# Kernel tuning notes

Measured on AMD Instinct MI355X. Metric: run time of the kernel, lower is better.

## Reference

```python
import jax, jax.numpy as jnp
import numpy as np

H = 256  # hidden_size
B = 8192  # batch
S = 1024  # seq_length


def setup_inputs() -> dict:
    key = jax.random.key(0)
    ks = jax.random.split(key, 12)
    lim_g = 1.0 / np.sqrt(1 + H)  # torch Linear default init bound, fan_in = 1+H
    lim_o = 1.0 / np.sqrt(H)
    def lin(k, out_dim, in_dim, lim):
        kw, kb = jax.random.split(k)
        W = jax.random.uniform(kw, (out_dim, in_dim), jnp.float32, -lim, lim)
        b = jax.random.uniform(kb, (out_dim,), jnp.float32, -lim, lim)
        return W, b
    Wf, bf = lin(ks[0], H, 1 + H, lim_g)
    Wi, bi = lin(ks[1], H, 1 + H, lim_g)
    Wc, bc = lin(ks[2], H, 1 + H, lim_g)
    Wo, bo = lin(ks[3], H, 1 + H, lim_g)
    Wout, bout = lin(ks[4], 1, H, lim_o)
    x = jax.random.normal(ks[5], (B, S), jnp.float32)
    return {"x": x, "Wf": Wf, "bf": bf, "Wi": Wi, "bi": bi,
            "Wc": Wc, "bc": bc, "Wo": Wo, "bo": bo,
            "Wout": Wout, "bout": bout}


def reference(x, Wf, bf, Wi, bi, Wc, bc, Wo, bo, Wout, bout):
    B_, S_ = x.shape
    H_ = Wf.shape[0]
    # Fuse the four gate linears into one GEMM per step (same math):
    Wall = jnp.concatenate([Wf, Wi, Wc, Wo], axis=0)      # [4H, 1+H]
    ball = jnp.concatenate([bf, bi, bc, bo], axis=0)      # [4H]

    def step(carry, xt):
        h, c = carry                                       # [B,H], [B,H]
        conc = jnp.concatenate([xt[:, None], h], axis=1)   # [B, 1+H]
        g = conc @ Wall.T + ball                           # [B, 4H]
        f, i, cs, o = jnp.split(g, 4, axis=1)
        c = jax.nn.sigmoid(f) * c + jax.nn.sigmoid(i) * jnp.tanh(cs)
        h = jax.nn.sigmoid(o) * jnp.tanh(c)
        return (h, c), None

    h0 = jnp.zeros((B_, H_), x.dtype)
    c0 = jnp.zeros((B_, H_), x.dtype)
    (h, _), _ = jax.lax.scan(step, (h0, c0), x.T)          # scan over seq axis
    out = h @ Wout.T + bout                                # [B, 1]
    return out.squeeze(-1)                                 # [B]
```

## Files before the change

### kernel.cpp

```cpp
#include <hip/hip_runtime.h>
#include <hip/hip_fp16.h>


typedef _Float16 f16x8 __attribute__((ext_vector_type(8)));
typedef float f32x4 __attribute__((ext_vector_type(4)));
typedef unsigned int u32;
typedef unsigned short u16;

#define WINT_OFF 0u
#define W0B_OFF  524288u
#define FLAG_OFF 528384u
#define PUB_OFF  1048576u

static __device__ __forceinline__ float fast_exp2(float x) {
#if __has_builtin(__builtin_amdgcn_exp2f)
  return __builtin_amdgcn_exp2f(x);
#else
  return exp2f(x);
#endif
}
static __device__ __forceinline__ float fast_rcp(float x) {
#if __has_builtin(__builtin_amdgcn_rcpf)
  return __builtin_amdgcn_rcpf(x);
#else
  return 1.0f / x;
#endif
}
static __device__ __forceinline__ float fsig(float x) {
  return fast_rcp(1.0f + fast_exp2(-1.44269504f * x));
}
static __device__ __forceinline__ float ftanh_(float x) {
  float e = fast_exp2(2.88539008f * x);
  return 1.0f - 2.0f * fast_rcp(e + 1.0f);
}
static __device__ __forceinline__ u16 f16b(float f) {
  union { _Float16 h; u16 u; } cv; cv.h = (_Float16)f; return cv.u;
}
static __device__ __forceinline__ float h2f(u16 u) {
  union { u16 u; _Float16 h; } cv; cv.u = u; return (float)cv.h;
}
static __device__ __forceinline__ u16* pub_base(u16* pub, int set, int par,
                                                int pid, int half) {
  return pub + ((size_t)(((set * 2 + par) * 128 + pid) * 2 + half) << 12);
}

__global__ void lstm_prep(const float* __restrict__ Wf, const float* __restrict__ Wi,
                          const float* __restrict__ Wc, const float* __restrict__ Wo,
                          const float* __restrict__ bf_, const float* __restrict__ bi_,
                          const float* __restrict__ bc_, const float* __restrict__ bo_,
                          u16* __restrict__ Wint, u32* __restrict__ w0b) {
  int n = blockIdx.x;
  int k = threadIdx.x;
  int g = n >> 8, j = n & 255;
  const float* Ws = (g == 0) ? Wf : (g == 1) ? Wi : (g == 2) ? Wc : Wo;
  Wint[n * 256 + k] = f16b(Ws[j * 257 + 1 + k]);
  if (k == 0) {
    const float* bs = (g == 0) ? bf_ : (g == 1) ? bi_ : (g == 2) ? bc_ : bo_;
    w0b[n] = (u32)f16b(Ws[j * 257]) | ((u32)f16b(bs[j]) << 16);
  }
}

__global__ void lstm_zero(uint4* __restrict__ pub4, uint4* __restrict__ flags4,
                          float* __restrict__ out, const float* __restrict__ bout) {
  int idx = blockIdx.x * 256 + threadIdx.x;
  uint4 z = uint4{0, 0, 0, 0};
  if (idx < 131072) pub4[idx] = z;
  else if (idx < 262144) pub4[idx + 131072] = z;
  else if (idx < 264192) flags4[idx - 262144] = z;
  else { int o = idx - 264192; if (o < 8192) out[o] = bout[0]; }
}

__global__ __launch_bounds__(512, 2) void lstm_main(
    const u16* __restrict__ Wint, const u32* __restrict__ w0b,
    const float* __restrict__ x, const float* __restrict__ Wout,
    float* __restrict__ out, u16* __restrict__ pub, int* __restrict__ flags) {

  __shared__ __align__(16) u16 stg[2][2][4096];

  const int tid  = threadIdx.x;
  const int wv   = tid >> 6;
  const int lane = tid & 63;
  const int l15  = lane & 15;
  const int quad = lane >> 4;
  const int B    = blockIdx.x;
  const int mi   = (B >> 3) & 1;
  const int peer = B ^ 8;
  const int pid  = (B & 7) | ((B >> 4) << 3);
  const int rows0 = pid * 64;

  f16x8 wfrag[4][8];
#pragma unroll
  for (int g = 0; g < 4; ++g)
#pragma unroll
    for (int hm = 0; hm < 2; ++hm)
#pragma unroll
      for (int ktl = 0; ktl < 4; ++ktl) {
        int kbase = (hm == 0 ? mi : 1 - mi) * 128 + ktl * 32;
        wfrag[g][hm * 4 + ktl] = *(const f16x8*)(Wint +
            (size_t)(g * 256 + mi * 128 + wv * 16 + l15) * 256 + kbase + quad * 8);
      }
  uint4 w0bv[4];
#pragma unroll
  for (int g = 0; g < 4; ++g)
    w0bv[g] = *(const uint4*)(w0b + g * 256 + mi * 128 + wv * 16 + quad * 4);

#pragma unroll
  for (int i = 0; i < 4; ++i) ((uint4*)stg)[tid + i * 512] = uint4{0, 0, 0, 0};

  float cst[2][2][4];
#pragma unroll
  for (int s = 0; s < 2; ++s)
#pragma unroll
    for (int bt = 0; bt < 2; ++bt)
#pragma unroll
      for (int r = 0; r < 4; ++r) cst[s][bt][r] = 0.0f;

  const float* xq = x + (size_t)rows0 * 1024;
  float xcur[2][2];
#pragma unroll
  for (int s = 0; s < 2; ++s)
#pragma unroll
    for (int bt = 0; bt < 2; ++bt)
      xcur[s][bt] = xq[(size_t)(s * 32 + bt * 16 + l15) * 1024];

  int* const myflag = flags + B * 32;
  int* const pfl    = flags + peer * 32;

  __syncthreads();

#pragma unroll 1
  for (int t = 0; t < 1024; ++t) {
#pragma unroll
    for (int s = 0; s < 2; ++s) {
      f32x4 acc[4][2];
#pragma unroll
      for (int g = 0; g < 4; ++g) {
        u32 pka[4] = {w0bv[g].x, w0bv[g].y, w0bv[g].z, w0bv[g].w};
#pragma unroll
        for (int r = 0; r < 4; ++r) {
          float w0f = h2f((u16)pka[r]), bsf = h2f((u16)(pka[r] >> 16));
          acc[g][0][r] = xcur[s][0] * w0f + bsf;
          acc[g][1][r] = xcur[s][1] * w0f + bsf;
        }
      }
#pragma unroll
      for (int bt = 0; bt < 2; ++bt)
        xcur[s][bt] = xq[(size_t)(s * 32 + bt * 16 + l15) * 1024 + ((t + 1) & 1023)];

#pragma unroll
      for (int hm = 0; hm < 2; ++hm)
#pragma unroll
        for (int ktl = 0; ktl < 4; ++ktl) {
          f16x8 bb[2];
#pragma unroll
          for (int bt = 0; bt < 2; ++bt) {
            int b = bt * 16 + l15;
            int cp = (ktl * 4 + quad) ^ (b & 15);
            bb[bt] = *(const f16x8*)(&stg[s][hm][0] + b * 128 + cp * 8);
          }
#pragma unroll
          for (int g = 0; g < 4; ++g)
#pragma unroll
            for (int bt = 0; bt < 2; ++bt)
              acc[g][bt] = __builtin_amdgcn_mfma_f32_16x16x32_f16(
                  wfrag[g][hm * 4 + ktl], bb[bt], acc[g][bt], 0, 0, 0);
        }

      const int tn = (s == 0) ? t : t + 1;
      if (tn < 1024) {
        while (__hip_atomic_load(pfl + (s ^ 1) * 16, __ATOMIC_RELAXED,
                                 __HIP_MEMORY_SCOPE_AGENT) < tn)
          __builtin_amdgcn_s_sleep(1);
        const u16* srcO = pub_base(pub, s ^ 1, tn & 1, pid, mi);
        const u16* srcP = pub_base(pub, s ^ 1, tn & 1, pid, 1 - mi);
        __builtin_amdgcn_global_load_lds(
            (const __attribute__((address_space(1))) u32*)(srcO + wv * 512 + lane * 8),
            (__attribute__((address_space(3))) u32*)(&stg[s ^ 1][0][wv * 512]), 16, 0, 0);
        __builtin_amdgcn_global_load_lds(
            (const __attribute__((address_space(1))) u32*)(srcP + wv * 512 + lane * 8),
            (__attribute__((address_space(3))) u32*)(&stg[s ^ 1][1][wv * 512]), 16, 0, 0);
      }

      u16* pb = pub_base(pub, s, (t + 1) & 1, pid, mi);
#pragma unroll
      for (int bt = 0; bt < 2; ++bt) {
        int b = bt * 16 + l15;
        u32 lo, hi;
        {
          float h0, h1, h2, h3;
#pragma unroll
          for (int r = 0; r < 4; ++r) {
            float fg = acc[0][bt][r], ig = acc[1][bt][r];
            float cg = acc[2][bt][r], og = acc[3][bt][r];
            float c_ = fsig(fg) * cst[s][bt][r] + fsig(ig) * ftanh_(cg);
            cst[s][bt][r] = c_;
            float hv = fsig(og) * ftanh_(c_);
            if (r == 0) h0 = hv; else if (r == 1) h1 = hv;
            else if (r == 2) h2 = hv; else h3 = hv;
          }
          lo = (u32)f16b(h0) | ((u32)f16b(h1) << 16);
          hi = (u32)f16b(h2) | ((u32)f16b(h3) << 16);
        }
        int c16 = wv * 2 + (quad >> 1);
        int cp  = c16 ^ (b & 15);
        *(uint2*)(pb + b * 128 + cp * 8 + (quad & 1) * 4) = uint2{lo, hi};
      }

      __syncthreads();
      if (tid == 0)
        __hip_atomic_store(myflag + s * 16, t + 1, __ATOMIC_RELAXED,
                           __HIP_MEMORY_SCOPE_AGENT);
    }
  }

  if (tid < 64) {
    int s = tid >> 5, b = tid & 31;
    const u16* pbase = pub_base(pub, s, 0, pid, mi);
    float a = 0.0f;
#pragma unroll
    for (int c = 0; c < 16; ++c) {
      f16x8 hv = *(const f16x8*)(pbase + b * 128 + ((c ^ (b & 15)) * 8));
#pragma unroll
      for (int e = 0; e < 8; ++e) a += (float)hv[e] * Wout[mi * 128 + c * 8 + e];
    }
    atomicAdd(&out[rows0 + s * 32 + b], a);
  }
}

extern "C" void kernel_launch(void* const* d_in, const int* in_sizes, int n_in,
                              void* d_out, int out_size, void* d_ws, size_t ws_size,
                              hipStream_t stream) {
  const float* x    = (const float*)d_in[0];
  const float* Wf   = (const float*)d_in[1];
  const float* bf_  = (const float*)d_in[2];
  const float* Wi   = (const float*)d_in[3];
  const float* bi_  = (const float*)d_in[4];
  const float* Wc   = (const float*)d_in[5];
  const float* bc_  = (const float*)d_in[6];
  const float* Wo   = (const float*)d_in[7];
  const float* bo_  = (const float*)d_in[8];
  const float* Wout = (const float*)d_in[9];
  const float* bout = (const float*)d_in[10];

  u16* Wint  = (u16*)((char*)d_ws + WINT_OFF);
  u32* w0b   = (u32*)((char*)d_ws + W0B_OFF);
  int* flags = (int*)((char*)d_ws + FLAG_OFF);
  u16* pub   = (u16*)((char*)d_ws + PUB_OFF);

  lstm_prep<<<1024, 256, 0, stream>>>(Wf, Wi, Wc, Wo, bf_, bi_, bc_, bo_, Wint, w0b);
  lstm_zero<<<1064, 256, 0, stream>>>((uint4*)pub, (uint4*)flags, (float*)d_out, bout);
  lstm_main<<<256, 512, 0, stream>>>(Wint, w0b, x, Wout, (float*)d_out, pub, flags);
}
```

Before: 4.928 ms.

## Split hidden units across four cooperating blocks instead of two

Each 64-row batch group is now handled by four blocks of 256 threads, each owning 64 hidden units, in place of two blocks of 512 threads owning 128. Each block waits on three peer flags and gathers the full hidden state from a shared publish buffer into LDS. The goal is to double the block count (512) so more CUs share the recurrent work. The cost is more cross-block synchronisation per step and more flag polling latency.

```diff
diff --git a/kernel.cpp b/kernel.cpp
--- a/kernel.cpp
+++ b/kernel.cpp
@@ -39,9 +39,8 @@
 static __device__ __forceinline__ float h2f(u16 u) {
   union { u16 u; _Float16 h; } cv; cv.u = u; return (float)cv.h;
 }
-static __device__ __forceinline__ u16* pub_base(u16* pub, int set, int par,
-                                                int pid, int half) {
-  return pub + ((size_t)(((set * 2 + par) * 128 + pid) * 2 + half) << 12);
+static __device__ __forceinline__ u16* pub_base(u16* pub, int set, int par, int qd) {
+  return pub + ((size_t)((set * 2 + par) * 128 + qd) << 13);
 }
 
 __global__ void lstm_prep(const float* __restrict__ Wf, const float* __restrict__ Wi,
@@ -66,16 +65,16 @@
   uint4 z = uint4{0, 0, 0, 0};
   if (idx < 131072) pub4[idx] = z;
   else if (idx < 262144) pub4[idx + 131072] = z;
-  else if (idx < 264192) flags4[idx - 262144] = z;
-  else { int o = idx - 264192; if (o < 8192) out[o] = bout[0]; }
-}
-
-__global__ __launch_bounds__(512, 2) void lstm_main(
+  else if (idx < 266240) flags4[idx - 262144] = z;
+  else { int o = idx - 266240; if (o < 8192) out[o] = bout[0]; }
+}
+
+__global__ __launch_bounds__(256, 2) void lstm_main(
     const u16* __restrict__ Wint, const u32* __restrict__ w0b,
     const float* __restrict__ x, const float* __restrict__ Wout,
     float* __restrict__ out, u16* __restrict__ pub, int* __restrict__ flags) {
 
-  __shared__ __align__(16) u16 stg[2][2][4096];
+  __shared__ __align__(16) u16 stg[2][4][2048];
 
   const int tid  = threadIdx.x;
   const int wv   = tid >> 6;
@@ -83,29 +82,26 @@
   const int l15  = lane & 15;
   const int quad = lane >> 4;
   const int B    = blockIdx.x;
-  const int mi   = (B >> 3) & 1;
-  const int peer = B ^ 8;
-  const int pid  = (B & 7) | ((B >> 4) << 3);
-  const int rows0 = pid * 64;
+  const int qi   = (B >> 3) & 3;
+  const int qd   = (B & 7) | ((B >> 5) << 3);
+  const int b0   = (qd & 7) | ((qd >> 3) << 5);
+  const int rows0 = qd * 64;
+  const int j0g  = qi * 64 + wv * 16;
 
   f16x8 wfrag[4][8];
 #pragma unroll
   for (int g = 0; g < 4; ++g)
 #pragma unroll
-    for (int hm = 0; hm < 2; ++hm)
-#pragma unroll
-      for (int ktl = 0; ktl < 4; ++ktl) {
-        int kbase = (hm == 0 ? mi : 1 - mi) * 128 + ktl * 32;
-        wfrag[g][hm * 4 + ktl] = *(const f16x8*)(Wint +
-            (size_t)(g * 256 + mi * 128 + wv * 16 + l15) * 256 + kbase + quad * 8);
-      }
+    for (int ks = 0; ks < 8; ++ks)
+      wfrag[g][ks] = *(const f16x8*)(Wint +
+          (size_t)(g * 256 + j0g + l15) * 256 + ks * 32 + quad * 8);
   uint4 w0bv[4];
 #pragma unroll
   for (int g = 0; g < 4; ++g)
-    w0bv[g] = *(const uint4*)(w0b + g * 256 + mi * 128 + wv * 16 + quad * 4);
-
-#pragma unroll
-  for (int i = 0; i < 4; ++i) ((uint4*)stg)[tid + i * 512] = uint4{0, 0, 0, 0};
+    w0bv[g] = *(const uint4*)(w0b + g * 256 + j0g + quad * 4);
+
+#pragma unroll
+  for (int i = 0; i < 8; ++i) ((uint4*)stg)[tid + i * 256] = uint4{0, 0, 0, 0};
 
   float cst[2][2][4];
 #pragma unroll
@@ -124,7 +120,10 @@
       xcur[s][bt] = xq[(size_t)(s * 32 + bt * 16 + l15) * 1024];
 
   int* const myflag = flags + B * 32;
-  int* const pfl    = flags + peer * 32;
+  int* pfl[3];
+#pragma unroll
+  for (int d = 0; d < 3; ++d)
+    pfl[d] = flags + (b0 + (((qi + d + 1) & 3) << 3)) * 32;
 
   __syncthreads();
 
@@ -148,40 +147,42 @@
         xcur[s][bt] = xq[(size_t)(s * 32 + bt * 16 + l15) * 1024 + ((t + 1) & 1023)];
 
 #pragma unroll
-      for (int hm = 0; hm < 2; ++hm)
-#pragma unroll
-        for (int ktl = 0; ktl < 4; ++ktl) {
-          f16x8 bb[2];
-#pragma unroll
-          for (int bt = 0; bt < 2; ++bt) {
-            int b = bt * 16 + l15;
-            int cp = (ktl * 4 + quad) ^ (b & 15);
-            bb[bt] = *(const f16x8*)(&stg[s][hm][0] + b * 128 + cp * 8);
-          }
-#pragma unroll
-          for (int g = 0; g < 4; ++g)
-#pragma unroll
-            for (int bt = 0; bt < 2; ++bt)
-              acc[g][bt] = __builtin_amdgcn_mfma_f32_16x16x32_f16(
-                  wfrag[g][hm * 4 + ktl], bb[bt], acc[g][bt], 0, 0, 0);
-        }
+      for (int ks = 0; ks < 8; ++ks) {
+        const u16* qimg = &stg[s][ks >> 1][0];
+        f16x8 bb[2];
+#pragma unroll
+        for (int bt = 0; bt < 2; ++bt) {
+          int b = bt * 16 + l15;
+          int c = (((ks & 1) * 4 + quad)) ^ (b & 7);
+          bb[bt] = *(const f16x8*)(qimg + b * 64 + c * 8);
+        }
+#pragma unroll
+        for (int g = 0; g < 4; ++g)
+#pragma unroll
+          for (int bt = 0; bt < 2; ++bt)
+            acc[g][bt] = __builtin_amdgcn_mfma_f32_16x16x32_f16(
+                wfrag[g][ks], bb[bt], acc[g][bt], 0, 0, 0);
+      }
 
       const int tn = (s == 0) ? t : t + 1;
       if (tn < 1024) {
-        while (__hip_atomic_load(pfl + (s ^ 1) * 16, __ATOMIC_RELAXED,
-                                 __HIP_MEMORY_SCOPE_AGENT) < tn)
-          __builtin_amdgcn_s_sleep(1);
-        const u16* srcO = pub_base(pub, s ^ 1, tn & 1, pid, mi);
-        const u16* srcP = pub_base(pub, s ^ 1, tn & 1, pid, 1 - mi);
-        __builtin_amdgcn_global_load_lds(
-            (const __attribute__((address_space(1))) u32*)(srcO + wv * 512 + lane * 8),
-            (__attribute__((address_space(3))) u32*)(&stg[s ^ 1][0][wv * 512]), 16, 0, 0);
-        __builtin_amdgcn_global_load_lds(
-            (const __attribute__((address_space(1))) u32*)(srcP + wv * 512 + lane * 8),
-            (__attribute__((address_space(3))) u32*)(&stg[s ^ 1][1][wv * 512]), 16, 0, 0);
-      }
-
-      u16* pb = pub_base(pub, s, (t + 1) & 1, pid, mi);
+#pragma unroll
+        for (int d = 0; d < 3; ++d)
+          while (__hip_atomic_load(pfl[d] + (s ^ 1) * 16, __ATOMIC_RELAXED,
+                                   __HIP_MEMORY_SCOPE_AGENT) < tn)
+            __builtin_amdgcn_s_sleep(1);
+        const u16* src = pub_base(pub, s ^ 1, tn & 1, qd);
+#pragma unroll
+        for (int i = 0; i < 4; ++i) {
+          int ch = (i * 4 + wv) * 64;
+          __builtin_amdgcn_global_load_lds(
+              (const __attribute__((address_space(1))) u32*)(src + (ch + lane) * 8),
+              (__attribute__((address_space(3))) u32*)(&stg[s ^ 1][0][0] + ch * 8),
+              16, 0, 0);
+        }
+      }
+
+      u16* pb = pub_base(pub, s, (t + 1) & 1, qd) + qi * 2048;
 #pragma unroll
       for (int bt = 0; bt < 2; ++bt) {
         int b = bt * 16 + l15;
@@ -201,9 +202,9 @@
           lo = (u32)f16b(h0) | ((u32)f16b(h1) << 16);
           hi = (u32)f16b(h2) | ((u32)f16b(h3) << 16);
         }
-        int c16 = wv * 2 + (quad >> 1);
-        int cp  = c16 ^ (b & 15);
-        *(uint2*)(pb + b * 128 + cp * 8 + (quad & 1) * 4) = uint2{lo, hi};
+        int jc = wv * 2 + (quad >> 1);
+        int c  = jc ^ (b & 7);
+        *(uint2*)(pb + b * 64 + c * 8 + (quad & 1) * 4) = uint2{lo, hi};
       }
 
       __syncthreads();
@@ -215,13 +216,13 @@
 
   if (tid < 64) {
     int s = tid >> 5, b = tid & 31;
-    const u16* pbase = pub_base(pub, s, 0, pid, mi);
+    const u16* pbase = pub_base(pub, s, 0, qd) + qi * 2048;
     float a = 0.0f;
 #pragma unroll
-    for (int c = 0; c < 16; ++c) {
-      f16x8 hv = *(const f16x8*)(pbase + b * 128 + ((c ^ (b & 15)) * 8));
-#pragma unroll
-      for (int e = 0; e < 8; ++e) a += (float)hv[e] * Wout[mi * 128 + c * 8 + e];
+    for (int c = 0; c < 8; ++c) {
+      f16x8 hv = *(const f16x8*)(pbase + b * 64 + ((c ^ (b & 7)) * 8));
+#pragma unroll
+      for (int e = 0; e < 8; ++e) a += (float)hv[e] * Wout[qi * 64 + c * 8 + e];
     }
     atomicAdd(&out[rows0 + s * 32 + b], a);
   }
@@ -248,6 +249,6 @@
   u16* pub   = (u16*)((char*)d_ws + PUB_OFF);
 
   lstm_prep<<<1024, 256, 0, stream>>>(Wf, Wi, Wc, Wo, bf_, bi_, bc_, bo_, Wint, w0b);
-  lstm_zero<<<1064, 256, 0, stream>>>((uint4*)pub, (uint4*)flags, (float*)d_out, bout);
-  lstm_main<<<256, 512, 0, stream>>>(Wint, w0b, x, Wout, (float*)d_out, pub, flags);
-}
+  lstm_zero<<<1072, 256, 0, stream>>>((uint4*)pub, (uint4*)flags, (float*)d_out, bout);
+  lstm_main<<<512, 256, 0, stream>>>(Wint, w0b, x, Wout, (float*)d_out, pub, flags);
+}
```

New measurement: 5.126 ms. 1.04x slower.

## Split batch into four 16-row substreams and overlap gate math with next MFMA

Applied to the files above, without the earlier changes.

Restructures the persistent LSTM kernel from two 32-row substreams to four 16-row substreams, rotating through them in a software pipeline. Each substep applies the activation and publishes h for the previous substream while the MFMAs for the current one are issued, so transcendental work overlaps matrix work. Published h is now stored as full 256-wide rows in one buffer instead of two halves, and each peer block fetches a single chunk per substep. The cost is four barriers and flag handshakes per timestep instead of two, more complex flag and buffer indexing, and a final epilogue substep.

```diff
diff --git a/kernel.cpp b/kernel.cpp
--- a/kernel.cpp
+++ b/kernel.cpp
@@ -38,10 +38,6 @@
 }
 static __device__ __forceinline__ float h2f(u16 u) {
   union { u16 u; _Float16 h; } cv; cv.u = u; return (float)cv.h;
-}
-static __device__ __forceinline__ u16* pub_base(u16* pub, int set, int par,
-                                                int pid, int half) {
-  return pub + ((size_t)(((set * 2 + par) * 128 + pid) * 2 + half) << 12);
 }
 
 __global__ void lstm_prep(const float* __restrict__ Wf, const float* __restrict__ Wi,
@@ -64,10 +60,11 @@
                           float* __restrict__ out, const float* __restrict__ bout) {
   int idx = blockIdx.x * 256 + threadIdx.x;
   uint4 z = uint4{0, 0, 0, 0};
-  if (idx < 131072) pub4[idx] = z;
-  else if (idx < 262144) pub4[idx + 131072] = z;
-  else if (idx < 264192) flags4[idx - 262144] = z;
-  else { int o = idx - 264192; if (o < 8192) out[o] = bout[0]; }
+  if (idx < 262144) {
+    int s = idx >> 16, off = idx & 65535;
+    pub4[(size_t)s * 131072 + off] = z;
+  } else if (idx < 266240) flags4[idx - 262144] = z;
+  else { int o = idx - 266240; if (o < 8192) out[o] = bout[0]; }
 }
 
 __global__ __launch_bounds__(512, 2) void lstm_main(
@@ -75,7 +72,7 @@
     const float* __restrict__ x, const float* __restrict__ Wout,
     float* __restrict__ out, u16* __restrict__ pub, int* __restrict__ flags) {
 
-  __shared__ __align__(16) u16 stg[2][2][4096];
+  __shared__ __align__(16) u16 stg[4][4096];
 
   const int tid  = threadIdx.x;
   const int wv   = tid >> 6;
@@ -87,144 +84,147 @@
   const int peer = B ^ 8;
   const int pid  = (B & 7) | ((B >> 4) << 3);
   const int rows0 = pid * 64;
+  const int j0w  = mi * 128 + wv * 16;
 
   f16x8 wfrag[4][8];
 #pragma unroll
   for (int g = 0; g < 4; ++g)
 #pragma unroll
-    for (int hm = 0; hm < 2; ++hm)
-#pragma unroll
-      for (int ktl = 0; ktl < 4; ++ktl) {
-        int kbase = (hm == 0 ? mi : 1 - mi) * 128 + ktl * 32;
-        wfrag[g][hm * 4 + ktl] = *(const f16x8*)(Wint +
-            (size_t)(g * 256 + mi * 128 + wv * 16 + l15) * 256 + kbase + quad * 8);
-      }
-  uint4 w0bv[4];
+    for (int ks = 0; ks < 8; ++ks)
+      wfrag[g][ks] = *(const f16x8*)(Wint +
+          (size_t)(g * 256 + j0w + l15) * 256 + ks * 32 + quad * 8);
+  float w0f[4][4], bsf[4][4];
 #pragma unroll
   for (int g = 0; g < 4; ++g)
-    w0bv[g] = *(const uint4*)(w0b + g * 256 + mi * 128 + wv * 16 + quad * 4);
+#pragma unroll
+    for (int r = 0; r < 4; ++r) {
+      u32 pk = w0b[g * 256 + j0w + quad * 4 + r];
+      w0f[g][r] = h2f((u16)pk); bsf[g][r] = h2f((u16)(pk >> 16));
+    }
 
 #pragma unroll
   for (int i = 0; i < 4; ++i) ((uint4*)stg)[tid + i * 512] = uint4{0, 0, 0, 0};
 
-  float cst[2][2][4];
-#pragma unroll
-  for (int s = 0; s < 2; ++s)
-#pragma unroll
-    for (int bt = 0; bt < 2; ++bt)
-#pragma unroll
-      for (int r = 0; r < 4; ++r) cst[s][bt][r] = 0.0f;
+  float cst[4][4];
+#pragma unroll
+  for (int s = 0; s < 4; ++s)
+#pragma unroll
+    for (int r = 0; r < 4; ++r) cst[s][r] = 0.0f;
 
   const float* xq = x + (size_t)rows0 * 1024;
-  float xcur[2][2];
-#pragma unroll
-  for (int s = 0; s < 2; ++s)
-#pragma unroll
-    for (int bt = 0; bt < 2; ++bt)
-      xcur[s][bt] = xq[(size_t)(s * 32 + bt * 16 + l15) * 1024];
-
-  int* const myflag = flags + B * 32;
-  int* const pfl    = flags + peer * 32;
+  float xcur[4];
+#pragma unroll
+  for (int s = 0; s < 4; ++s) xcur[s] = xq[(size_t)(s * 16 + l15) * 1024];
+
+  f32x4 accA[4], accB[4];
 
   __syncthreads();
+
+#define SUBSTEP(S, ACC, PREV, SP, TP1, GUARD, SN, TN, DGUARD)                     \
+  do {                                                                            \
+    f16x8 bb0[4], bb1[4];                                                         \
+    _Pragma("unroll")                                                             \
+    for (int ks = 0; ks < 4; ++ks) {                                              \
+      int c = (ks * 4 + quad) ^ (l15 & 7);                                        \
+      bb0[ks] = *(const f16x8*)(&stg[S][0] + l15 * 256 + c * 8);                  \
+    }                                                                             \
+                    \
+    if (GUARD) {                                                                  \
+      float hv4[4];                                                               \
+      _Pragma("unroll")                                                           \
+      for (int r = 0; r < 4; ++r) {                                               \
+        float fg = PREV[0][r], ig = PREV[1][r];                                   \
+        float cg = PREV[2][r], og = PREV[3][r];                                   \
+        float c_ = fsig(fg) * cst[SP][r] + fsig(ig) * ftanh_(cg);                 \
+        cst[SP][r] = c_;                                                          \
+        hv4[r] = fsig(og) * ftanh_(c_);                                           \
+      }                                                                           \
+      u32 lo = (u32)f16b(hv4[0]) | ((u32)f16b(hv4[1]) << 16);                     \
+      u32 hi = (u32)f16b(hv4[2]) | ((u32)f16b(hv4[3]) << 16);                     \
+      u16* pb = pub + ((size_t)(((SP) * 2 + ((TP1) & 1)) * 128 + pid)) * 4096;    \
+      int cpub = (mi * 16 + wv * 2 + (quad >> 1)) ^ (l15 & 7);                    \
+      *(uint2*)(pb + l15 * 256 + cpub * 8 + (quad & 1) * 4) = uint2{lo, hi};      \
+    }                                                                             \
+                                                       \
+    _Pragma("unroll")                                                             \
+    for (int g = 0; g < 4; ++g)                                                   \
+      _Pragma("unroll")                                                           \
+      for (int r = 0; r < 4; ++r)                                                 \
+        ACC[g][r] = xcur[S] * w0f[g][r] + bsf[g][r];                              \
+    xcur[S] = xq[(size_t)((S) * 16 + l15) * 1024 + ((t + 1) & 1023)];             \
+                                                                 \
+    _Pragma("unroll")                                                             \
+    for (int ks = 0; ks < 4; ++ks)                                                \
+      _Pragma("unroll")                                                           \
+      for (int g = 0; g < 4; ++g)                                                 \
+        ACC[g] = __builtin_amdgcn_mfma_f32_16x16x32_f16(                          \
+            wfrag[g][ks], bb0[ks], ACC[g], 0, 0, 0);                              \
+    _Pragma("unroll")                                                             \
+    for (int ks = 4; ks < 8; ++ks) {                                              \
+      int c = (ks * 4 + quad) ^ (l15 & 7);                                        \
+      bb1[ks - 4] = *(const f16x8*)(&stg[S][0] + l15 * 256 + c * 8);              \
+    }                                                                             \
+    _Pragma("unroll")                                                             \
+    for (int ks = 4; ks < 8; ++ks)                                                \
+      _Pragma("unroll")                                                           \
+      for (int g = 0; g < 4; ++g)                                                 \
+        ACC[g] = __builtin_amdgcn_mfma_f32_16x16x32_f16(                          \
+            wfrag[g][ks], bb1[ks - 4], ACC[g], 0, 0, 0);                          \
+                     \
+    if (DGUARD) {                                                                 \
+      while (__hip_atomic_load(flags + (peer * 4 + (SN)) * 16, __ATOMIC_RELAXED,  \
+                               __HIP_MEMORY_SCOPE_AGENT) < (TN))                  \
+        __builtin_amdgcn_s_sleep(1);                                              \
+      const u16* src = pub + ((size_t)(((SN) * 2 + ((TN) & 1)) * 128 + pid)) * 4096; \
+      __builtin_amdgcn_global_load_lds(                                           \
+          (const __attribute__((address_space(1))) u32*)(src + wv * 512 + lane * 8), \
+          (__attribute__((address_space(3))) u32*)(&stg[SN][0] + wv * 512), 16, 0, 0); \
+    }                                                                             \
+    __syncthreads();                                                              \
+    if (tid == 0 && (GUARD))                                                      \
+      __hip_atomic_store(flags + (B * 4 + (SP)) * 16, (TP1), __ATOMIC_RELAXED,    \
+                         __HIP_MEMORY_SCOPE_AGENT);                               \
+  } while (0)
 
 #pragma unroll 1
   for (int t = 0; t < 1024; ++t) {
-#pragma unroll
-    for (int s = 0; s < 2; ++s) {
-      f32x4 acc[4][2];
-#pragma unroll
-      for (int g = 0; g < 4; ++g) {
-        u32 pka[4] = {w0bv[g].x, w0bv[g].y, w0bv[g].z, w0bv[g].w};
-#pragma unroll
-        for (int r = 0; r < 4; ++r) {
-          float w0f = h2f((u16)pka[r]), bsf = h2f((u16)(pka[r] >> 16));
-          acc[g][0][r] = xcur[s][0] * w0f + bsf;
-          acc[g][1][r] = xcur[s][1] * w0f + bsf;
-        }
-      }
-#pragma unroll
-      for (int bt = 0; bt < 2; ++bt)
-        xcur[s][bt] = xq[(size_t)(s * 32 + bt * 16 + l15) * 1024 + ((t + 1) & 1023)];
-
-#pragma unroll
-      for (int hm = 0; hm < 2; ++hm)
-#pragma unroll
-        for (int ktl = 0; ktl < 4; ++ktl) {
-          f16x8 bb[2];
-#pragma unroll
-          for (int bt = 0; bt < 2; ++bt) {
-            int b = bt * 16 + l15;
-            int cp = (ktl * 4 + quad) ^ (b & 15);
-            bb[bt] = *(const f16x8*)(&stg[s][hm][0] + b * 128 + cp * 8);
-          }
-#pragma unroll
-          for (int g = 0; g < 4; ++g)
-#pragma unroll
-            for (int bt = 0; bt < 2; ++bt)
-              acc[g][bt] = __builtin_amdgcn_mfma_f32_16x16x32_f16(
-                  wfrag[g][hm * 4 + ktl], bb[bt], acc[g][bt], 0, 0, 0);
-        }
-
-      const int tn = (s == 0) ? t : t + 1;
-      if (tn < 1024) {
-        while (__hip_atomic_load(pfl + (s ^ 1) * 16, __ATOMIC_RELAXED,
-                                 __HIP_MEMORY_SCOPE_AGENT) < tn)
-          __builtin_amdgcn_s_sleep(1);
-        const u16* srcO = pub_base(pub, s ^ 1, tn & 1, pid, mi);
-        const u16* srcP = pub_base(pub, s ^ 1, tn & 1, pid, 1 - mi);
-        __builtin_amdgcn_global_load_lds(
-            (const __attribute__((address_space(1))) u32*)(srcO + wv * 512 + lane * 8),
-            (__attribute__((address_space(3))) u32*)(&stg[s ^ 1][0][wv * 512]), 16, 0, 0);
-        __builtin_amdgcn_global_load_lds(
-            (const __attribute__((address_space(1))) u32*)(srcP + wv * 512 + lane * 8),
-            (__attribute__((address_space(3))) u32*)(&stg[s ^ 1][1][wv * 512]), 16, 0, 0);
-      }
-
-      u16* pb = pub_base(pub, s, (t + 1) & 1, pid, mi);
-#pragma unroll
-      for (int bt = 0; bt < 2; ++bt) {
-        int b = bt * 16 + l15;
-        u32 lo, hi;
-        {
-          float h0, h1, h2, h3;
-#pragma unroll
-          for (int r = 0; r < 4; ++r) {
-            float fg = acc[0][bt][r], ig = acc[1][bt][r];
-            float cg = acc[2][bt][r], og = acc[3][bt][r];
-            float c_ = fsig(fg) * cst[s][bt][r] + fsig(ig) * ftanh_(cg);
-            cst[s][bt][r] = c_;
-            float hv = fsig(og) * ftanh_(c_);
-            if (r == 0) h0 = hv; else if (r == 1) h1 = hv;
-            else if (r == 2) h2 = hv; else h3 = hv;
-          }
-          lo = (u32)f16b(h0) | ((u32)f16b(h1) << 16);
-          hi = (u32)f16b(h2) | ((u32)f16b(h3) << 16);
-        }
-        int c16 = wv * 2 + (quad >> 1);
-        int cp  = c16 ^ (b & 15);
-        *(uint2*)(pb + b * 128 + cp * 8 + (quad & 1) * 4) = uint2{lo, hi};
-      }
-
-      __syncthreads();
-      if (tid == 0)
-        __hip_atomic_store(myflag + s * 16, t + 1, __ATOMIC_RELAXED,
-                           __HIP_MEMORY_SCOPE_AGENT);
+    SUBSTEP(0, accA, accB, 3, t,     (t > 0), 1, t,     true);
+    SUBSTEP(1, accB, accA, 0, t + 1, true,    2, t,     true);
+    SUBSTEP(2, accA, accB, 1, t + 1, true,    3, t,     true);
+    SUBSTEP(3, accB, accA, 2, t + 1, true,    0, t + 1, (t < 1023));
+  }
+
+  {
+    float hv4[4];
+#pragma unroll
+    for (int r = 0; r < 4; ++r) {
+      float fg = accB[0][r], ig = accB[1][r];
+      float cg = accB[2][r], og = accB[3][r];
+      float c_ = fsig(fg) * cst[3][r] + fsig(ig) * ftanh_(cg);
+      hv4[r] = fsig(og) * ftanh_(c_);
     }
-  }
+    u32 lo = (u32)f16b(hv4[0]) | ((u32)f16b(hv4[1]) << 16);
+    u32 hi = (u32)f16b(hv4[2]) | ((u32)f16b(hv4[3]) << 16);
+    u16* pb = pub + ((size_t)((3 * 2 + 0) * 128 + pid)) * 4096;
+    int cpub = (mi * 16 + wv * 2 + (quad >> 1)) ^ (l15 & 7);
+    *(uint2*)(pb + l15 * 256 + cpub * 8 + (quad & 1) * 4) = uint2{lo, hi};
+  }
+  __syncthreads();
 
   if (tid < 64) {
-    int s = tid >> 5, b = tid & 31;
-    const u16* pbase = pub_base(pub, s, 0, pid, mi);
+    int s = tid >> 4, b = tid & 15;
+    const u16* pbase = pub + ((size_t)((s * 2 + 0) * 128 + pid)) * 4096;
     float a = 0.0f;
 #pragma unroll
-    for (int c = 0; c < 16; ++c) {
-      f16x8 hv = *(const f16x8*)(pbase + b * 128 + ((c ^ (b & 15)) * 8));
-#pragma unroll
-      for (int e = 0; e < 8; ++e) a += (float)hv[e] * Wout[mi * 128 + c * 8 + e];
+    for (int lc = 0; lc < 16; ++lc) {
+      int cp = (mi * 16 + lc) ^ (b & 7);
+      f16x8 hv = *(const f16x8*)(pbase + b * 256 + cp * 8);
+#pragma unroll
+      for (int e = 0; e < 8; ++e) a += (float)hv[e] * Wout[mi * 128 + lc * 8 + e];
     }
-    atomicAdd(&out[rows0 + s * 32 + b], a);
-  }
+    atomicAdd(&out[rows0 + s * 16 + b], a);
+  }
+#undef SUBSTEP
 }
 
 extern "C" void kernel_launch(void* const* d_in, const int* in_sizes, int n_in,
@@ -248,6 +248,6 @@
   u16* pub   = (u16*)((char*)d_ws + PUB_OFF);
 
   lstm_prep<<<1024, 256, 0, stream>>>(Wf, Wi, Wc, Wo, bf_, bi_, bc_, bo_, Wint, w0b);
-  lstm_zero<<<1064, 256, 0, stream>>>((uint4*)pub, (uint4*)flags, (float*)d_out, bout);
+  lstm_zero<<<1072, 256, 0, stream>>>((uint4*)pub, (uint4*)flags, (float*)d_out, bout);
   lstm_main<<<256, 512, 0, stream>>>(Wint, w0b, x, Wout, (float*)d_out, pub, flags);
 }
```

Result: slower. 6.395 ms (+29.8%).

## Software-pipeline LSTM sub-batches and split peer wait around the local-half MFMAs

Applied to the files above, without the earlier changes.

Restructures the per-step loop so each phase first runs the MFMAs for the locally produced half of h, then applies the previous sub-batch's gate activations and publishes them. Only after that does it wait on per-wave peer flags and fetch the peer's half into LDS, then finish the remaining MFMAs. Own h is written straight to LDS as well as global, so only the peer half is reloaded. Activations are merged to share reciprocals, and the input weights and biases are moved to LDS as floats. The aim is to hide cross-block flag latency behind useful compute, at the cost of more complex synchronization (8 flags polled per wait) and more accumulator registers.

```diff
diff --git a/kernel.cpp b/kernel.cpp
--- a/kernel.cpp
+++ b/kernel.cpp
@@ -25,13 +25,6 @@
 #else
   return 1.0f / x;
 #endif
-}
-static __device__ __forceinline__ float fsig(float x) {
-  return fast_rcp(1.0f + fast_exp2(-1.44269504f * x));
-}
-static __device__ __forceinline__ float ftanh_(float x) {
-  float e = fast_exp2(2.88539008f * x);
-  return 1.0f - 2.0f * fast_rcp(e + 1.0f);
 }
 static __device__ __forceinline__ u16 f16b(float f) {
   union { _Float16 h; u16 u; } cv; cv.h = (_Float16)f; return cv.u;
@@ -76,6 +69,7 @@
     float* __restrict__ out, u16* __restrict__ pub, int* __restrict__ flags) {
 
   __shared__ __align__(16) u16 stg[2][2][4096];
+  __shared__ __align__(16) float lw0f[512], lbsf[512];
 
   const int tid  = threadIdx.x;
   const int wv   = tid >> 6;
@@ -87,6 +81,7 @@
   const int peer = B ^ 8;
   const int pid  = (B & 7) | ((B >> 4) << 3);
   const int rows0 = pid * 64;
+  const int j0w  = mi * 128 + wv * 16;
 
   f16x8 wfrag[4][8];
 #pragma unroll
@@ -97,13 +92,13 @@
       for (int ktl = 0; ktl < 4; ++ktl) {
         int kbase = (hm == 0 ? mi : 1 - mi) * 128 + ktl * 32;
         wfrag[g][hm * 4 + ktl] = *(const f16x8*)(Wint +
-            (size_t)(g * 256 + mi * 128 + wv * 16 + l15) * 256 + kbase + quad * 8);
+            (size_t)(g * 256 + j0w + l15) * 256 + kbase + quad * 8);
       }
-  uint4 w0bv[4];
-#pragma unroll
-  for (int g = 0; g < 4; ++g)
-    w0bv[g] = *(const uint4*)(w0b + g * 256 + mi * 128 + wv * 16 + quad * 4);
-
+  {
+    u32 pk = w0b[(tid >> 7) * 256 + mi * 128 + (tid & 127)];
+    lw0f[tid] = h2f((u16)pk);
+    lbsf[tid] = h2f((u16)(pk >> 16));
+  }
 #pragma unroll
   for (int i = 0; i < 4; ++i) ((uint4*)stg)[tid + i * 512] = uint4{0, 0, 0, 0};
 
@@ -123,105 +118,159 @@
     for (int bt = 0; bt < 2; ++bt)
       xcur[s][bt] = xq[(size_t)(s * 32 + bt * 16 + l15) * 1024];
 
-  int* const myflag = flags + B * 32;
-  int* const pfl    = flags + peer * 32;
+  f32x4 acc0[4][2], acc1[4][2];
 
   __syncthreads();
+
+#define PHASE(S, ACC, ACCP, FSTEP, DO_EW)                                         \
+  {                                                                               \
+    const int sd_ = 1 - (S);                                                      \
+                                            \
+    _Pragma("unroll")                                                             \
+    for (int g = 0; g < 4; ++g) {                                                 \
+      f32x4 wv4_ = *(const f32x4*)&lw0f[g * 128 + wv * 16 + quad * 4];            \
+      f32x4 bv4_ = *(const f32x4*)&lbsf[g * 128 + wv * 16 + quad * 4];            \
+      _Pragma("unroll")                                                           \
+      for (int r = 0; r < 4; ++r) {                                               \
+        ACC[g][0][r] = xcur[S][0] * wv4_[r] + bv4_[r];                            \
+        ACC[g][1][r] = xcur[S][1] * wv4_[r] + bv4_[r];                            \
+      }                                                                           \
+    }                                                                             \
+                                            \
+    _Pragma("unroll")                                                             \
+    for (int ks = 0; ks < 2; ++ks) {                                              \
+      const u16* bs_ = &stg[S][0][0];                                             \
+      int cp_ = (ks * 4 + quad) ^ l15;                                            \
+      f16x8 ba_ = *(const f16x8*)(bs_ + l15 * 128 + cp_ * 8);                     \
+      f16x8 bb_ = *(const f16x8*)(bs_ + (16 + l15) * 128 + cp_ * 8);              \
+      _Pragma("unroll")                                                           \
+      for (int g = 0; g < 4; ++g) {                                               \
+        ACC[g][0] = __builtin_amdgcn_mfma_f32_16x16x32_f16(wfrag[g][ks], ba_,     \
+                                                           ACC[g][0], 0, 0, 0);   \
+        ACC[g][1] = __builtin_amdgcn_mfma_f32_16x16x32_f16(wfrag[g][ks], bb_,     \
+                                                           ACC[g][1], 0, 0, 0);   \
+      }                                                                           \
+    }                                                                             \
+         \
+    if (DO_EW) {                                                                  \
+      u16* pb_ = pub_base(pub, sd_, (FSTEP) & 1, pid, mi);                        \
+      u16* ls_ = &stg[sd_][0][0];                                                 \
+      _Pragma("unroll")                                                           \
+      for (int bt = 0; bt < 2; ++bt) {                                            \
+        int brow_ = bt * 16 + l15;                                                \
+        float h4_[4];                                                             \
+        _Pragma("unroll")                                                         \
+        for (int r = 0; r < 4; ++r) {                                             \
+          float fg_ = ACCP[0][bt][r], ig_ = ACCP[1][bt][r];                       \
+          float cg_ = ACCP[2][bt][r], og_ = ACCP[3][bt][r];                       \
+          float ef_ = fast_exp2(-1.44269504f * fg_);                              \
+          float ei_ = fast_exp2(-1.44269504f * ig_);                              \
+          float eg_ = fast_exp2(2.88539008f * cg_);                               \
+          float eo_ = fast_exp2(-1.44269504f * og_);                              \
+          float c_ = cst[sd_][bt][r] * fast_rcp(1.0f + ef_) +                     \
+                     (eg_ - 1.0f) * fast_rcp((1.0f + ei_) * (eg_ + 1.0f));        \
+          cst[sd_][bt][r] = c_;                                                   \
+          float ec_ = fast_exp2(2.88539008f * c_);                                \
+          h4_[r] = (ec_ - 1.0f) * fast_rcp((1.0f + eo_) * (ec_ + 1.0f));          \
+        }                                                                         \
+        u32 lo_ = (u32)f16b(h4_[0]) | ((u32)f16b(h4_[1]) << 16);                  \
+        u32 hi_ = (u32)f16b(h4_[2]) | ((u32)f16b(h4_[3]) << 16);                  \
+        int off_ = brow_ * 128 + ((wv * 2 + (quad >> 1)) ^ l15) * 8 +             \
+                   (quad & 1) * 4;                                                \
+        *(uint2*)(pb_ + off_) = uint2{lo_, hi_};                                  \
+        *(uint2*)(ls_ + off_) = uint2{lo_, hi_};                                  \
+      }                                                                           \
+    }                                                                             \
+                    \
+    __builtin_amdgcn_s_waitcnt(0x0f70);                        \
+    if ((DO_EW) && lane == 0)                                                     \
+      __hip_atomic_store(flags + ((B) * 2 + sd_) * 16 + wv, (FSTEP),              \
+                         __ATOMIC_RELAXED, __HIP_MEMORY_SCOPE_AGENT);             \
+          \
+    {                                                                             \
+      const int* pfl_ = flags + (peer * 2 + sd_) * 16;                            \
+      for (;;) {                                                                  \
+        int mn_ = 0x7fffffff;                                                     \
+        _Pragma("unroll")                                                         \
+        for (int d = 0; d < 8; ++d) {                                             \
+          int v_ = __hip_atomic_load(pfl_ + d, __ATOMIC_RELAXED,                  \
+                                     __HIP_MEMORY_SCOPE_AGENT);                   \
+          mn_ = mn_ < v_ ? mn_ : v_;                                              \
+        }                                                                         \
+        if (mn_ >= (FSTEP)) break;                                                \
+        __builtin_amdgcn_s_sleep(1);                                              \
+      }                                                                           \
+      const u16* src_ = pub_base(pub, sd_, (FSTEP) & 1, pid, 1 - mi);             \
+      __builtin_amdgcn_global_load_lds(                                           \
+          (const __attribute__((address_space(1))) u32*)(src_ + wv * 512 +        \
+                                                         lane * 8),               \
+          (__attribute__((address_space(3))) u32*)(&stg[sd_][1][wv * 512]),       \
+          16, 0, 0);                                                              \
+    }                                                                             \
+                                                          \
+    _Pragma("unroll")                                                             \
+    for (int ks = 2; ks < 8; ++ks) {                                              \
+      const u16* bs_ = &stg[S][ks >> 2][0];                                       \
+      int cp_ = ((ks & 3) * 4 + quad) ^ l15;                                      \
+      f16x8 ba_ = *(const f16x8*)(bs_ + l15 * 128 + cp_ * 8);                     \
+      f16x8 bb_ = *(const f16x8*)(bs_ + (16 + l15) * 128 + cp_ * 8);              \
+      _Pragma("unroll")                                                           \
+      for (int g = 0; g < 4; ++g) {                                               \
+        ACC[g][0] = __builtin_amdgcn_mfma_f32_16x16x32_f16(wfrag[g][ks], ba_,     \
+                                                           ACC[g][0], 0, 0, 0);   \
+        ACC[g][1] = __builtin_amdgcn_mfma_f32_16x16x32_f16(wfrag[g][ks], bb_,     \
+                                                           ACC[g][1], 0, 0, 0);   \
+      }                                                                           \
+    }                                                                             \
+                                                     \
+    xcur[S][0] = xq[(size_t)((S) * 32 + l15) * 1024 + ((t + 1) & 1023)];          \
+    xcur[S][1] = xq[(size_t)((S) * 32 + 16 + l15) * 1024 + ((t + 1) & 1023)];     \
+    __syncthreads();                    \
+  }
 
 #pragma unroll 1
   for (int t = 0; t < 1024; ++t) {
-#pragma unroll
-    for (int s = 0; s < 2; ++s) {
-      f32x4 acc[4][2];
-#pragma unroll
-      for (int g = 0; g < 4; ++g) {
-        u32 pka[4] = {w0bv[g].x, w0bv[g].y, w0bv[g].z, w0bv[g].w};
-#pragma unroll
-        for (int r = 0; r < 4; ++r) {
-          float w0f = h2f((u16)pka[r]), bsf = h2f((u16)(pka[r] >> 16));
-          acc[g][0][r] = xcur[s][0] * w0f + bsf;
-          acc[g][1][r] = xcur[s][1] * w0f + bsf;
-        }
+    PHASE(0, acc0, acc1, t, (t > 0));
+    PHASE(1, acc1, acc0, (t + 1), 1);
+  }
+#undef PHASE
+
+  {
+    u16* ls = &stg[1][0][0];
+#pragma unroll
+    for (int bt = 0; bt < 2; ++bt) {
+      int brow = bt * 16 + l15;
+      float h4[4];
+#pragma unroll
+      for (int r = 0; r < 4; ++r) {
+        float fg = acc1[0][bt][r], ig = acc1[1][bt][r];
+        float cg = acc1[2][bt][r], og = acc1[3][bt][r];
+        float ef = fast_exp2(-1.44269504f * fg);
+        float ei = fast_exp2(-1.44269504f * ig);
+        float eg = fast_exp2(2.88539008f * cg);
+        float eo = fast_exp2(-1.44269504f * og);
+        float c_ = cst[1][bt][r] * fast_rcp(1.0f + ef) +
+                   (eg - 1.0f) * fast_rcp((1.0f + ei) * (eg + 1.0f));
+        float ec = fast_exp2(2.88539008f * c_);
+        h4[r] = (ec - 1.0f) * fast_rcp((1.0f + eo) * (ec + 1.0f));
       }
-#pragma unroll
-      for (int bt = 0; bt < 2; ++bt)
-        xcur[s][bt] = xq[(size_t)(s * 32 + bt * 16 + l15) * 1024 + ((t + 1) & 1023)];
-
-#pragma unroll
-      for (int hm = 0; hm < 2; ++hm)
-#pragma unroll
-        for (int ktl = 0; ktl < 4; ++ktl) {
-          f16x8 bb[2];
-#pragma unroll
-          for (int bt = 0; bt < 2; ++bt) {
-            int b = bt * 16 + l15;
-            int cp = (ktl * 4 + quad) ^ (b & 15);
-            bb[bt] = *(const f16x8*)(&stg[s][hm][0] + b * 128 + cp * 8);
-          }
-#pragma unroll
-          for (int g = 0; g < 4; ++g)
-#pragma unroll
-            for (int bt = 0; bt < 2; ++bt)
-              acc[g][bt] = __builtin_amdgcn_mfma_f32_16x16x32_f16(
-                  wfrag[g][hm * 4 + ktl], bb[bt], acc[g][bt], 0, 0, 0);
-        }
-
-      const int tn = (s == 0) ? t : t + 1;
-      if (tn < 1024) {
-        while (__hip_atomic_load(pfl + (s ^ 1) * 16, __ATOMIC_RELAXED,
-                                 __HIP_MEMORY_SCOPE_AGENT) < tn)
-          __builtin_amdgcn_s_sleep(1);
-        const u16* srcO = pub_base(pub, s ^ 1, tn & 1, pid, mi);
-        const u16* srcP = pub_base(pub, s ^ 1, tn & 1, pid, 1 - mi);
-        __builtin_amdgcn_global_load_lds(
-            (const __attribute__((address_space(1))) u32*)(srcO + wv * 512 + lane * 8),
-            (__attribute__((address_space(3))) u32*)(&stg[s ^ 1][0][wv * 512]), 16, 0, 0);
-        __builtin_amdgcn_global_load_lds(
-            (const __attribute__((address_space(1))) u32*)(srcP + wv * 512 + lane * 8),
-            (__attribute__((address_space(3))) u32*)(&stg[s ^ 1][1][wv * 512]), 16, 0, 0);
-      }
-
-      u16* pb = pub_base(pub, s, (t + 1) & 1, pid, mi);
-#pragma unroll
-      for (int bt = 0; bt < 2; ++bt) {
-        int b = bt * 16 + l15;
-        u32 lo, hi;
-        {
-          float h0, h1, h2, h3;
-#pragma unroll
-          for (int r = 0; r < 4; ++r) {
-            float fg = acc[0][bt][r], ig = acc[1][bt][r];
-            float cg = acc[2][bt][r], og = acc[3][bt][r];
-            float c_ = fsig(fg) * cst[s][bt][r] + fsig(ig) * ftanh_(cg);
-            cst[s][bt][r] = c_;
-            float hv = fsig(og) * ftanh_(c_);
-            if (r == 0) h0 = hv; else if (r == 1) h1 = hv;
-            else if (r == 2) h2 = hv; else h3 = hv;
-          }
-          lo = (u32)f16b(h0) | ((u32)f16b(h1) << 16);
-          hi = (u32)f16b(h2) | ((u32)f16b(h3) << 16);
-        }
-        int c16 = wv * 2 + (quad >> 1);
-        int cp  = c16 ^ (b & 15);
-        *(uint2*)(pb + b * 128 + cp * 8 + (quad & 1) * 4) = uint2{lo, hi};
-      }
-
-      __syncthreads();
-      if (tid == 0)
-        __hip_atomic_store(myflag + s * 16, t + 1, __ATOMIC_RELAXED,
-                           __HIP_MEMORY_SCOPE_AGENT);
+      u32 lo = (u32)f16b(h4[0]) | ((u32)f16b(h4[1]) << 16);
+      u32 hi = (u32)f16b(h4[2]) | ((u32)f16b(h4[3]) << 16);
+      int off = brow * 128 + ((wv * 2 + (quad >> 1)) ^ l15) * 8 + (quad & 1) * 4;
+      *(uint2*)(ls + off) = uint2{lo, hi};
     }
   }
+  __syncthreads();
 
   if (tid < 64) {
     int s = tid >> 5, b = tid & 31;
-    const u16* pbase = pub_base(pub, s, 0, pid, mi);
+    const u16* img = &stg[s][0][0];
     float a = 0.0f;
 #pragma unroll
-    for (int c = 0; c < 16; ++c) {
-      f16x8 hv = *(const f16x8*)(pbase + b * 128 + ((c ^ (b & 15)) * 8));
-#pragma unroll
-      for (int e = 0; e < 8; ++e) a += (float)hv[e] * Wout[mi * 128 + c * 8 + e];
+    for (int lc = 0; lc < 16; ++lc) {
+      f16x8 hv = *(const f16x8*)(img + b * 128 + ((lc ^ (b & 15)) * 8));
+#pragma unroll
+      for (int e = 0; e < 8; ++e) a += (float)hv[e] * Wout[mi * 128 + lc * 8 + e];
     }
     atomicAdd(&out[rows0 + s * 32 + b], a);
   }
```

Result: slower. 12.19 ms (+147.4%).
